# Performance work log

Hardware: AMD Instinct MI355X
Metric: run time of the kernel (lower is better)

The kernel has to match this reference:

```python
import jax, jax.numpy as jnp
import numpy as np

N_NODES = 100000
N_EDGES = 800000
F_IN = 300
F_PROJ = 256
HIDDEN = 256
F2 = 128
OUT = 4
NEG_SLOPE = 0.2
BN_EPS = 1e-5


def setup_inputs() -> dict:
    key = jax.random.key(0)
    ks = jax.random.split(key, 20)
    def g(k, shape, scale=0.05):
        return jax.random.normal(k, shape, dtype=jnp.float32) * scale
    return {
        "x": jax.random.normal(ks[0], (N_NODES, F_IN), dtype=jnp.float32),
        "edge_index": jax.random.randint(ks[1], (2, N_EDGES), 0, N_NODES),
        "lin_w": g(ks[2], (F_IN, F_PROJ)), "lin_b": jnp.zeros((F_PROJ,), jnp.float32),
        "w1_src": g(ks[3], (F_PROJ, HIDDEN)), "w1_dst": g(ks[4], (F_PROJ, HIDDEN)),
        "a1_src": g(ks[5], (HIDDEN,)), "a1_dst": g(ks[6], (HIDDEN,)),
        "b1": jnp.zeros((HIDDEN,), jnp.float32),
        "w2_src": g(ks[7], (HIDDEN, F2)), "w2_dst": g(ks[8], (HIDDEN, F2)),
        "a2_src": g(ks[9], (F2,)), "a2_dst": g(ks[10], (F2,)),
        "b2": jnp.zeros((F2,), jnp.float32),
        "fc1_w": g(ks[11], (F2, 64)), "fc1_b": jnp.zeros((64,), jnp.float32),
        "bn_g": jnp.ones((64,), jnp.float32), "bn_b": jnp.zeros((64,), jnp.float32),
        "fc2_w": g(ks[12], (64, OUT)), "fc2_b": jnp.zeros((OUT,), jnp.float32),
    }


def gat_conv(x, src, dst, w_src, w_dst, att_src, att_dst, bias, n):
    # PyG GATConv, heads=1: separate src/dst linear, additive attention, LeakyReLU,
    # per-destination segment softmax, weighted scatter-add aggregation.
    h_src = x @ w_src                      # [N, C]
    h_dst = x @ w_dst                      # [N, C]
    a_s = h_src @ att_src                  # [N]
    a_d = h_dst @ att_dst                  # [N]
    e = jax.nn.leaky_relu(a_s[src] + a_d[dst], NEG_SLOPE)  # [E]
    m = jax.ops.segment_max(e, dst, num_segments=n)
    w = jnp.exp(e - m[dst])
    denom = jax.ops.segment_sum(w, dst, num_segments=n)
    alpha = w / (denom[dst] + 1e-16)       # [E]
    out = jax.ops.segment_sum(h_src[src] * alpha[:, None], dst, num_segments=n)
    return out + bias


def reference(x, edge_index, lin_w, lin_b, w1_src, w1_dst, a1_src, a1_dst, b1,
              w2_src, w2_dst, a2_src, a2_dst, b2, fc1_w, fc1_b, bn_g, bn_b,
              fc2_w, fc2_b):
    n = x.shape[0]
    loops = jnp.arange(n)
    src = jnp.concatenate([edge_index[0], loops])  # add_self_loops=True (PyG default)
    dst = jnp.concatenate([edge_index[1], loops])
    h = jax.nn.relu(x @ lin_w + lin_b)             # node-type Linear(-1, 256) + relu
    h = jax.nn.relu(gat_conv(h, src, dst, w1_src, w1_dst, a1_src, a1_dst, b1, n))
    h = jax.nn.relu(gat_conv(h, src, dst, w2_src, w2_dst, a2_src, a2_dst, b2, n))
    h = h @ fc1_w + fc1_b
    mu = jnp.mean(h, axis=0)
    var = jnp.var(h, axis=0)
    h = (h - mu) * jax.lax.rsqrt(var + BN_EPS) * bn_g + bn_b
    h = jax.nn.relu(h)
    h = h @ fc2_w + fc2_b
    return jax.nn.log_softmax(h, axis=-1)
```

## Files before the change

### kernel.cpp

```cpp
#include <hip/hip_runtime.h>
#include <hip/hip_bf16.h>
#include <cmath>

#define NN 100000
#define NE 800000
#define ETOT (NE + NN)
#define MP 100096

#define SCHUNK 512
#define NBLK ((NN + SCHUNK - 1) / SCHUNK)

typedef __attribute__((ext_vector_type(8))) short bf16x8;
typedef __attribute__((ext_vector_type(4))) float f32x4;

__device__ inline void gl_lds16(const void* g, void* l) {
    __builtin_amdgcn_global_load_lds(
        (const __attribute__((address_space(1))) void*)g,
        (__attribute__((address_space(3))) void*)l, 16, 0, 0);
}

__device__ inline ushort f2bf(float f) {
    __hip_bfloat16 b = __float2bfloat16(f);
    return *(ushort*)&b;
}
__device__ inline uint pk2(float a, float b) {
    return (uint)f2bf(a) | ((uint)f2bf(b) << 16);
}

__global__ __launch_bounds__(256)
void mfma_gemm(const __hip_bfloat16* __restrict__ Abf,
               const __hip_bfloat16* __restrict__ Btbf,
               const float* __restrict__ bias, void* __restrict__ out,
               const float* __restrict__ dotv, float* __restrict__ dotout,
               float* __restrict__ stats,
               int Kp, int ldc, int Mstore, int Nstore, int flags)
{
    __shared__ __align__(16) short As[128 * 32];
    __shared__ __align__(16) short Bs[128 * 32];
    const short* A  = (const short*)Abf;
    const short* Bt = (const short*)Btbf;

    const int tid  = threadIdx.x;
    const int lane = tid & 63;
    const int wv   = tid >> 6;
    const int wr   = (wv >> 1) * 64;
    const int wc   = (wv & 1) * 64;
    const int quad = lane >> 4;
    const int l16  = lane & 15;
    const long bm = (long)blockIdx.x * 128;
    const long bn = (long)blockIdx.y * 128;

    const int r0 = tid >> 2;
    const int c0 = (tid & 3) ^ ((r0 >> 1) & 3);
    const int r1 = r0 + 64;
    const int c1 = (tid & 3) ^ ((r1 >> 1) & 3);
    const short* a_g0 = A + (bm + r0) * (long)Kp + c0 * 8;
    const short* a_g1 = A + (bm + r1) * (long)Kp + c1 * 8;
    const short* b_g0 = Bt + (bn + r0) * (long)Kp + c0 * 8;
    const short* b_g1 = Bt + (bn + r1) * (long)Kp + c1 * 8;
    short* a_l0 = &As[tid * 8];
    short* a_l1 = &As[(tid + 256) * 8];
    short* b_l0 = &Bs[tid * 8];
    short* b_l1 = &Bs[(tid + 256) * 8];

    f32x4 acc[4][4] = {};
    const int xr = (quad ^ ((l16 >> 1) & 3)) * 8;

    for (int k0 = 0; k0 < Kp; k0 += 32) {
        gl_lds16(a_g0 + k0, a_l0);
        gl_lds16(a_g1 + k0, a_l1);
        gl_lds16(b_g0 + k0, b_l0);
        gl_lds16(b_g1 + k0, b_l1);
        __syncthreads();

        bf16x8 af[4], bf[4];
#pragma unroll
        for (int i = 0; i < 4; i++)
            af[i] = *(const bf16x8*)&As[(wr + i * 16 + l16) * 32 + xr];
#pragma unroll
        for (int j = 0; j < 4; j++)
            bf[j] = *(const bf16x8*)&Bs[(wc + j * 16 + l16) * 32 + xr];
#pragma unroll
        for (int i = 0; i < 4; i++)
#pragma unroll
            for (int j = 0; j < 4; j++)
                acc[i][j] = __builtin_amdgcn_mfma_f32_16x16x32_bf16(
                    af[i], bf[j], acc[i][j], 0, 0, 0);
        __syncthreads();
    }

    __hip_bfloat16* outb = (__hip_bfloat16*)out;
    float* outf = (float*)out;
    float dp[16];
    float sv[4], sv2[4];
#pragma unroll
    for (int t = 0; t < 16; t++) dp[t] = 0.f;
#pragma unroll
    for (int j = 0; j < 4; j++) { sv[j] = 0.f; sv2[j] = 0.f; }

#pragma unroll
    for (int i = 0; i < 4; i++) {
        long row_base = bm + wr + i * 16 + quad * 4;
#pragma unroll
        for (int j = 0; j < 4; j++) {
            long col = bn + wc + j * 16 + l16;
            if (col >= Nstore) continue;
            float bv = bias ? bias[col] : 0.f;
            float dv = dotout ? dotv[col] : 0.f;
#pragma unroll
            for (int r = 0; r < 4; r++) {
                long row = row_base + r;
                float v = acc[i][j][r] + bv;
                if (flags & 1) v = fmaxf(v, 0.f);
                dp[i * 4 + r] = fmaf(v, dv, dp[i * 4 + r]);
                if (row >= Mstore) continue;
                if (flags & 4) { sv[j] += v; sv2[j] += v * v; }
                if (flags & 2) outb[row * ldc + col] = __float2bfloat16(v);
                else           outf[row * ldc + col] = v;
            }
        }
    }

    if (dotout) {
#pragma unroll
        for (int t = 0; t < 16; t++) {
            float s = dp[t];
            s += __shfl_xor(s, 1); s += __shfl_xor(s, 2);
            s += __shfl_xor(s, 4); s += __shfl_xor(s, 8);
            if (l16 == 0) {
                long row = bm + wr + (t >> 2) * 16 + quad * 4 + (t & 3);
                if (row < Mstore) atomicAdd(&dotout[row], s);
            }
        }
    }

    if (flags & 4) {
#pragma unroll
        for (int j = 0; j < 4; j++) {
            float s = sv[j], s2 = sv2[j];
            s  += __shfl_xor(s, 16);  s  += __shfl_xor(s, 32);
            s2 += __shfl_xor(s2, 16); s2 += __shfl_xor(s2, 32);
            if (quad == 0) {
                long col = bn + wc + j * 16 + l16;
                if (col < Nstore) {
                    atomicAdd(&stats[col], s);
                    atomicAdd(&stats[64 + col], s2);
                }
            }
        }
    }
}

__global__ __launch_bounds__(256)
void cast_x_vec(const float* __restrict__ x, __hip_bfloat16* __restrict__ xb)
{
    const int idx = blockIdx.x * 256 + threadIdx.x;
    if (idx >= MP * 40) return;
    const int row = idx / 40;
    const int c8  = (idx % 40) * 8;
    uint4 v;
    if (row < NN && c8 + 8 <= 300) {
        const float* xp = x + (size_t)row * 300 + c8;
        float4 f0 = *(const float4*)xp;
        float4 f1 = *(const float4*)(xp + 4);
        v.x = pk2(f0.x, f0.y); v.y = pk2(f0.z, f0.w);
        v.z = pk2(f1.x, f1.y); v.w = pk2(f1.z, f1.w);
    } else {
        float f[8];
#pragma unroll
        for (int k = 0; k < 8; k++)
            f[k] = (row < NN && c8 + k < 300) ? x[(size_t)row * 300 + c8 + k] : 0.f;
        v.x = pk2(f[0], f[1]); v.y = pk2(f[2], f[3]);
        v.z = pk2(f[4], f[5]); v.w = pk2(f[6], f[7]);
    }
    *(uint4*)((ushort*)xb + (size_t)row * 320 + c8) = v;
}

__device__ inline void castT_one(const float* __restrict__ w,
                                 __hip_bfloat16* __restrict__ wt,
                                 int K, int N, int Kp, int idx)
{
    int n = idx / Kp, k = idx % Kp;
    float v = (n < N && k < K) ? w[(size_t)k * N + n] : 0.f;
    wt[idx] = __float2bfloat16(v);
}

__global__ __launch_bounds__(256)
void prep_small(const float* __restrict__ lin_w, const float* __restrict__ w1_src,
                const float* __restrict__ w2_src, const float* __restrict__ fc1_w,
                const float* __restrict__ w1_dst, const float* __restrict__ a1_dst,
                const float* __restrict__ w2_dst, const float* __restrict__ a2_dst,
                __hip_bfloat16* __restrict__ wlinT, __hip_bfloat16* __restrict__ w1T,
                __hip_bfloat16* __restrict__ w2T, __hip_bfloat16* __restrict__ fc1T,
                float* __restrict__ vvec1, float* __restrict__ vvec2)
{
    const int b = blockIdx.x;
    const int tid = threadIdx.x;
    if (b < 320) {
        castT_one(lin_w, wlinT, 300, 256, 320, b * 256 + tid);
    } else if (b < 576) {
        castT_one(w1_src, w1T, 256, 256, 256, (b - 320) * 256 + tid);
    } else if (b < 704) {
        castT_one(w2_src, w2T, 256, 128, 256, (b - 576) * 256 + tid);
    } else if (b < 768) {
        castT_one(fc1_w, fc1T, 128, 64, 128, (b - 704) * 256 + tid);
    } else if (b == 768) {
        float s = 0.f;
        for (int j = 0; j < 256; j++) s = fmaf(w1_dst[(size_t)tid * 256 + j], a1_dst[j], s);
        vvec1[tid] = s;
    } else {
        float s = 0.f;
        for (int j = 0; j < 128; j++) s = fmaf(w2_dst[(size_t)tid * 128 + j], a2_dst[j], s);
        vvec2[tid] = s;
    }
}

__global__ void count_edges(const int* __restrict__ ei, int* __restrict__ counts)
{
    int e = blockIdx.x * blockDim.x + threadIdx.x;
    if (e >= ETOT) return;
    int d = (e < NE) ? ei[NE + e] : (e - NE);
    atomicAdd(&counts[d], 1);
}

__global__ __launch_bounds__(256)
void scan_partial(const int* __restrict__ counts, int* __restrict__ blk)
{
    __shared__ int sh[256];
    const int tid = threadIdx.x;
    const int base = blockIdx.x * SCHUNK + tid * 2;
    int c0 = (base < NN)     ? counts[base]     : 0;
    int c1 = (base + 1 < NN) ? counts[base + 1] : 0;
    sh[tid] = c0 + c1;
    __syncthreads();
    for (int off = 128; off; off >>= 1) {
        if (tid < off) sh[tid] += sh[tid + off];
        __syncthreads();
    }
    if (tid == 0) blk[blockIdx.x] = sh[0];
}

__global__ __launch_bounds__(256)
void scan_blocks(int* __restrict__ blk)
{
    __shared__ int sh[256];
    const int tid = threadIdx.x;
    int v = (tid < NBLK) ? blk[tid] : 0;
    sh[tid] = v;
    __syncthreads();
    for (int off = 1; off < 256; off <<= 1) {
        int u = (tid >= off) ? sh[tid - off] : 0;
        __syncthreads();
        sh[tid] += u;
        __syncthreads();
    }
    if (tid < NBLK) blk[tid] = sh[tid] - v;
}

__global__ __launch_bounds__(256)
void scan_fill(const int* __restrict__ counts, const int* __restrict__ blk,
               int* __restrict__ row_ptr, int* __restrict__ cursor)
{
    __shared__ int sh[256];
    const int tid = threadIdx.x;
    const int i0 = blockIdx.x * SCHUNK + tid * 2;
    int c0 = (i0 < NN)     ? counts[i0]     : 0;
    int c1 = (i0 + 1 < NN) ? counts[i0 + 1] : 0;
    int s = c0 + c1;
    sh[tid] = s;
    __syncthreads();
    for (int off = 1; off < 256; off <<= 1) {
        int u = (tid >= off) ? sh[tid - off] : 0;
        __syncthreads();
        sh[tid] += u;
        __syncthreads();
    }
    int pre = sh[tid] - s + blk[blockIdx.x];
    if (i0 < NN)     { row_ptr[i0] = pre;          cursor[i0] = pre; }
    if (i0 + 1 < NN) { row_ptr[i0 + 1] = pre + c0; cursor[i0 + 1] = pre + c0; }
    if (blockIdx.x == 0 && tid == 0) row_ptr[NN] = ETOT;
}

__global__ void fill_edges(const int* __restrict__ ei, int* __restrict__ cursor,
                           int* __restrict__ csr_src)
{
    int e = blockIdx.x * blockDim.x + threadIdx.x;
    if (e >= ETOT) return;
    int s, d;
    if (e < NE) { s = ei[e]; d = ei[NE + e]; }
    else        { s = e - NE; d = s; }
    int pos = atomicAdd(&cursor[d], 1);
    csr_src[pos] = s;
}

template<int LPN>
__global__ __launch_bounds__(256)
void gat_agg_wave(const __hip_bfloat16* __restrict__ hsrc,
                  const float* __restrict__ a_s,
                  const float* __restrict__ a_d,
                  const int* __restrict__ row_ptr,
                  const int* __restrict__ csr_src,
                  const float* __restrict__ bias,
                  __hip_bfloat16* __restrict__ outh,
                  const float* __restrict__ dotv,
                  float* __restrict__ dotout)
{
    const int C = LPN * 4;
    const int NPB = 256 / LPN;
    __shared__ __align__(16) float2 ws_sh[NPB][LPN];

    const int tid  = threadIdx.x;
    const int slot = tid / LPN;
    const int sub  = tid % LPN;
    const int n = blockIdx.x * NPB + slot;
    if (n >= NN) return;

    const int start = row_ptr[n];
    const int deg = row_ptr[n + 1] - start;
    const float a_dn = a_d[n];
    const ushort* hp = (const ushort*)hsrc;

    float S = 0.f;
    float acc0 = 0.f, acc1 = 0.f, acc2 = 0.f, acc3 = 0.f;

    for (int c0 = 0; c0 < deg; c0 += LPN) {
        const int cnt = min(LPN, deg - c0);
        int sj = 0; float w = 0.f;
        if (sub < cnt) {
            sj = csr_src[start + c0 + sub];
            float t = a_s[sj] + a_dn;
            t = (t >= 0.f) ? t : 0.2f * t;
            w = __expf(t);
        }
        S += w;
        ws_sh[slot][sub] = make_float2(w, __int_as_float(sj));

        const int cnt8 = (cnt + 7) & ~7;
        const ushort* hpl = hp + sub * 4;
        for (int j = 0; j < cnt8; j += 8) {
            float4 p0 = *(const float4*)&ws_sh[slot][j];
            float4 p1 = *(const float4*)&ws_sh[slot][j + 2];
            float4 p2 = *(const float4*)&ws_sh[slot][j + 4];
            float4 p3 = *(const float4*)&ws_sh[slot][j + 6];
            uint2 u0 = *(const uint2*)(hpl + (size_t)__float_as_int(p0.y) * C);
            uint2 u1 = *(const uint2*)(hpl + (size_t)__float_as_int(p0.w) * C);
            uint2 u2 = *(const uint2*)(hpl + (size_t)__float_as_int(p1.y) * C);
            uint2 u3 = *(const uint2*)(hpl + (size_t)__float_as_int(p1.w) * C);
            uint2 u4 = *(const uint2*)(hpl + (size_t)__float_as_int(p2.y) * C);
            uint2 u5 = *(const uint2*)(hpl + (size_t)__float_as_int(p2.w) * C);
            uint2 u6 = *(const uint2*)(hpl + (size_t)__float_as_int(p3.y) * C);
            uint2 u7 = *(const uint2*)(hpl + (size_t)__float_as_int(p3.w) * C);
#define ACC4(W, U) \
            acc0 = fmaf(W, __uint_as_float(U.x << 16), acc0); \
            acc1 = fmaf(W, __uint_as_float(U.x & 0xffff0000u), acc1); \
            acc2 = fmaf(W, __uint_as_float(U.y << 16), acc2); \
            acc3 = fmaf(W, __uint_as_float(U.y & 0xffff0000u), acc3);
            ACC4(p0.x, u0) ACC4(p0.z, u1) ACC4(p1.x, u2) ACC4(p1.z, u3)
            ACC4(p2.x, u4) ACC4(p2.z, u5) ACC4(p3.x, u6) ACC4(p3.z, u7)
#undef ACC4
        }
    }

#pragma unroll
    for (int off = LPN / 2; off; off >>= 1) S += __shfl_xor(S, off);

    float inv = 1.f / (S + 1e-16f);
    const float4 b4 = *(const float4*)&bias[sub * 4];
    float o0 = fmaxf(acc0 * inv + b4.x, 0.f);
    float o1 = fmaxf(acc1 * inv + b4.y, 0.f);
    float o2 = fmaxf(acc2 * inv + b4.z, 0.f);
    float o3 = fmaxf(acc3 * inv + b4.w, 0.f);

    ushort4 v;
    v.x = f2bf(o0); v.y = f2bf(o1); v.z = f2bf(o2); v.w = f2bf(o3);
    *(ushort4*)((ushort*)outh + (size_t)n * C + sub * 4) = v;

    if (dotout) {
        const float4 d4 = *(const float4*)&dotv[sub * 4];
        float dp = o0 * d4.x + o1 * d4.y + o2 * d4.z + o3 * d4.w;
#pragma unroll
        for (int off = LPN / 2; off; off >>= 1) dp += __shfl_xor(dp, off);
        if (sub == 0) dotout[n] = dp;
    }
}

__global__ void bn_finalize(const float* __restrict__ stats,
                            const float* __restrict__ g, const float* __restrict__ b,
                            float* __restrict__ ss)
{
    int c = threadIdx.x;
    float mu = stats[c] / (float)NN;
    float var = stats[64 + c] / (float)NN - mu * mu;
    float rs = rsqrtf(var + 1e-5f);
    float sc = rs * g[c];
    ss[c] = sc;
    ss[64 + c] = b[c] - mu * sc;
}

__global__ __launch_bounds__(256)
void final_head(const float* __restrict__ h3, const float* __restrict__ ss,
                const float* __restrict__ fc2_w, const float* __restrict__ fc2_b,
                float* __restrict__ out)
{
    int lane = threadIdx.x & 63;
    int n = blockIdx.x * 4 + (threadIdx.x >> 6);
    if (n >= NN) return;
    float y = h3[(size_t)n * 64 + lane];
    y = fmaxf(y * ss[lane] + ss[64 + lane], 0.f);
    float z[4];
#pragma unroll
    for (int o = 0; o < 4; o++) {
        float p = y * fc2_w[lane * 4 + o];
#pragma unroll
        for (int off = 32; off; off >>= 1) p += __shfl_xor(p, off);
        z[o] = p + fc2_b[o];
    }
    float mx = fmaxf(fmaxf(z[0], z[1]), fmaxf(z[2], z[3]));
    float lse = mx + logf(expf(z[0] - mx) + expf(z[1] - mx) +
                          expf(z[2] - mx) + expf(z[3] - mx));
    if (lane < 4) out[(size_t)n * 4 + lane] = z[lane] - lse;
}

extern "C" void kernel_launch(void* const* d_in, const int* in_sizes, int n_in,
                              void* d_out, int out_size, void* d_ws, size_t ws_size,
                              hipStream_t stream)
{
    const float* x      = (const float*)d_in[0];
    const int*   ei     = (const int*)d_in[1];
    const float* lin_w  = (const float*)d_in[2];
    const float* lin_b  = (const float*)d_in[3];
    const float* w1_src = (const float*)d_in[4];
    const float* w1_dst = (const float*)d_in[5];
    const float* a1_src = (const float*)d_in[6];
    const float* a1_dst = (const float*)d_in[7];
    const float* b1     = (const float*)d_in[8];
    const float* w2_src = (const float*)d_in[9];
    const float* w2_dst = (const float*)d_in[10];
    const float* a2_src = (const float*)d_in[11];
    const float* a2_dst = (const float*)d_in[12];
    const float* b2     = (const float*)d_in[13];
    const float* fc1_w  = (const float*)d_in[14];
    const float* fc1_b  = (const float*)d_in[15];
    const float* bn_g   = (const float*)d_in[16];
    const float* bn_b   = (const float*)d_in[17];
    const float* fc2_w  = (const float*)d_in[18];
    const float* fc2_b  = (const float*)d_in[19];
    float* out = (float*)d_out;

    char* p = (char*)d_ws;
    auto alloc = [&](size_t bytes) { char* r = p; p += (bytes + 255) & ~(size_t)255; return r; };
    char* R1 = alloc((size_t)MP * 320 * 2);
    char* R2 = alloc((size_t)MP * 256 * 2);
    char* R3 = alloc((size_t)MP * 256 * 2);
    __hip_bfloat16* wlinT = (__hip_bfloat16*)alloc(256 * 320 * 2);
    __hip_bfloat16* w1T   = (__hip_bfloat16*)alloc(256 * 256 * 2);
    __hip_bfloat16* w2T   = (__hip_bfloat16*)alloc(128 * 256 * 2);
    __hip_bfloat16* fc1T  = (__hip_bfloat16*)alloc(128 * 128 * 2);
    float* avec  = (float*)alloc((size_t)NN * 4 * 4 + 512);
    float* aS1 = avec;
    float* aD1 = avec + NN;
    float* aS2 = avec + 2 * (size_t)NN;
    float* aD2 = avec + 3 * (size_t)NN;
    float* stats = avec + 4 * (size_t)NN;
    float* vvec1 = (float*)alloc(256 * 4);
    float* vvec2 = (float*)alloc(256 * 4);
    float* ss    = (float*)alloc(128 * 4);
    int* row_ptr = (int*)alloc((size_t)(NN + 1) * 4);
    int* cursor  = (int*)alloc((size_t)(NN + 1) * 4);
    int* counts  = (int*)alloc((size_t)NN * 4);
    int* blk     = (int*)alloc(256 * 4);
    int* csr_src = (int*)alloc((size_t)ETOT * 4);

    __hip_bfloat16* x_bf  = (__hip_bfloat16*)R1;
    __hip_bfloat16* hsrc1 = (__hip_bfloat16*)R1;
    __hip_bfloat16* h0    = (__hip_bfloat16*)R2;
    __hip_bfloat16* hsrc2 = (__hip_bfloat16*)R2;
    __hip_bfloat16* h2    = (__hip_bfloat16*)(R2 + (size_t)MP * 128 * 2);
    __hip_bfloat16* h1    = (__hip_bfloat16*)R3;
    float*          h3    = (float*)R3;

    const int eb = (ETOT + 255) / 256;
    const int MB = MP / 128;

    hipMemsetAsync(avec, 0, sizeof(float) * NN * 4 + 512, stream);

    hipMemsetAsync(counts, 0, sizeof(int) * NN, stream);
    count_edges<<<eb, 256, 0, stream>>>(ei, counts);
    scan_partial<<<NBLK, 256, 0, stream>>>(counts, blk);
    scan_blocks<<<1, 256, 0, stream>>>(blk);
    scan_fill<<<NBLK, 256, 0, stream>>>(counts, blk, row_ptr, cursor);
    fill_edges<<<eb, 256, 0, stream>>>(ei, cursor, csr_src);

    cast_x_vec<<<(MP * 40 + 255) / 256, 256, 0, stream>>>(x, x_bf);
    prep_small<<<770, 256, 0, stream>>>(lin_w, w1_src, w2_src, fc1_w,
                                        w1_dst, a1_dst, w2_dst, a2_dst,
                                        wlinT, w1T, w2T, fc1T, vvec1, vvec2);

    mfma_gemm<<<dim3(MB, 2), 256, 0, stream>>>(x_bf, wlinT, lin_b, h0,
                                               vvec1, aD1, nullptr, 320, 256, NN, 256, 3);

    mfma_gemm<<<dim3(MB, 2), 256, 0, stream>>>(h0, w1T, nullptr, hsrc1,
                                               a1_src, aS1, nullptr, 256, 256, NN, 256, 2);
    gat_agg_wave<64><<<(NN + 3) / 4, 256, 0, stream>>>(hsrc1, aS1, aD1, row_ptr,
                                                       csr_src, b1, h1, vvec2, aD2);

    mfma_gemm<<<dim3(MB, 1), 256, 0, stream>>>(h1, w2T, nullptr, hsrc2,
                                               a2_src, aS2, nullptr, 256, 128, NN, 128, 2);
    gat_agg_wave<32><<<(NN + 7) / 8, 256, 0, stream>>>(hsrc2, aS2, aD2, row_ptr,
                                                       csr_src, b2, h2, nullptr, nullptr);

    mfma_gemm<<<dim3(MB, 1), 256, 0, stream>>>(h2, fc1T, fc1_b, h3,
                                               nullptr, nullptr, stats, 128, 64, NN, 64, 4);
    bn_finalize<<<1, 64, 0, stream>>>(stats, bn_g, bn_b, ss);
    final_head<<<(NN + 3) / 4, 256, 0, stream>>>(h3, ss, fc2_w, fc2_b, out);
}
```

Measured before the change: 699.4 us.

## Restructure GEMM to stage only B panels in LDS and read A directly

Replaces the 128x128x32 LDS-tiled GEMM with a panel kernel. It loads a 128-row by 128-K slice of the weight matrix into LDS with an XOR swizzle, and each wave reads its 32 rows of A straight from global memory into registers. The goal is fewer barriers per K step and no LDS staging of the large activation matrix. In exchange, A reads become uncoalesced per-lane 16-byte global loads, and LDS use grows to 32KB, which may reduce occupancy.

```diff
diff --git a/kernel.cpp b/kernel.cpp
--- a/kernel.cpp
+++ b/kernel.cpp
@@ -28,91 +28,84 @@
 }
 
 __global__ __launch_bounds__(256)
-void mfma_gemm(const __hip_bfloat16* __restrict__ Abf,
-               const __hip_bfloat16* __restrict__ Btbf,
-               const float* __restrict__ bias, void* __restrict__ out,
-               const float* __restrict__ dotv, float* __restrict__ dotout,
-               float* __restrict__ stats,
-               int Kp, int ldc, int Mstore, int Nstore, int flags)
-{
-    __shared__ __align__(16) short As[128 * 32];
-    __shared__ __align__(16) short Bs[128 * 32];
+void gemm_panel(const __hip_bfloat16* __restrict__ Abf,
+                const __hip_bfloat16* __restrict__ Btbf,
+                const float* __restrict__ bias, void* __restrict__ out,
+                const float* __restrict__ dotv, float* __restrict__ dotout,
+                float* __restrict__ stats,
+                int Kp, int ldc, int Mstore, int Nstore, int flags)
+{
+    __shared__ __align__(16) short Bs[128 * 128];
     const short* A  = (const short*)Abf;
     const short* Bt = (const short*)Btbf;
 
     const int tid  = threadIdx.x;
     const int lane = tid & 63;
     const int wv   = tid >> 6;
-    const int wr   = (wv >> 1) * 64;
-    const int wc   = (wv & 1) * 64;
     const int quad = lane >> 4;
     const int l16  = lane & 15;
     const long bm = (long)blockIdx.x * 128;
     const long bn = (long)blockIdx.y * 128;
 
-    const int r0 = tid >> 2;
-    const int c0 = (tid & 3) ^ ((r0 >> 1) & 3);
-    const int r1 = r0 + 64;
-    const int c1 = (tid & 3) ^ ((r1 >> 1) & 3);
-    const short* a_g0 = A + (bm + r0) * (long)Kp + c0 * 8;
-    const short* a_g1 = A + (bm + r1) * (long)Kp + c1 * 8;
-    const short* b_g0 = Bt + (bn + r0) * (long)Kp + c0 * 8;
-    const short* b_g1 = Bt + (bn + r1) * (long)Kp + c1 * 8;
-    short* a_l0 = &As[tid * 8];
-    short* a_l1 = &As[(tid + 256) * 8];
-    short* b_l0 = &Bs[tid * 8];
-    short* b_l1 = &Bs[(tid + 256) * 8];
-
-    f32x4 acc[4][4] = {};
-    const int xr = (quad ^ ((l16 >> 1) & 3)) * 8;
-
-    for (int k0 = 0; k0 < Kp; k0 += 32) {
-        gl_lds16(a_g0 + k0, a_l0);
-        gl_lds16(a_g1 + k0, a_l1);
-        gl_lds16(b_g0 + k0, b_l0);
-        gl_lds16(b_g1 + k0, b_l1);
+    f32x4 acc[2][8] = {};
+
+    const short* a_row0 = A + (bm + wv * 32 + l16) * (long)Kp;
+    const short* a_row1 = a_row0 + 16 * (long)Kp;
+
+    for (int k0 = 0; k0 < Kp; k0 += 128) {
+        const int nc   = min(16, (Kp - k0) >> 3);
+        const int mask = nc - 1;
+        const int sh   = (nc == 16) ? 4 : 3;
+
+        if (k0 > 0) __syncthreads();
+        const int slots = 128 * nc;
+        for (int i = 0; i < slots; i += 256) {
+            int s = i + tid;
+            int row = s >> sh;
+            int cslot = s & mask;
+            int gc = cslot ^ (row & mask);
+            gl_lds16(Bt + (bn + row) * (long)Kp + k0 + gc * 8, &Bs[s * 8]);
+        }
         __syncthreads();
 
-        bf16x8 af[4], bf[4];
-#pragma unroll
-        for (int i = 0; i < 4; i++)
-            af[i] = *(const bf16x8*)&As[(wr + i * 16 + l16) * 32 + xr];
-#pragma unroll
-        for (int j = 0; j < 4; j++)
-            bf[j] = *(const bf16x8*)&Bs[(wc + j * 16 + l16) * 32 + xr];
-#pragma unroll
-        for (int i = 0; i < 4; i++)
-#pragma unroll
-            for (int j = 0; j < 4; j++)
-                acc[i][j] = __builtin_amdgcn_mfma_f32_16x16x32_bf16(
-                    af[i], bf[j], acc[i][j], 0, 0, 0);
-        __syncthreads();
+        const int nkk = nc >> 2;
+        const int cxor = l16 & mask;
+#pragma unroll 4
+        for (int kk = 0; kk < nkk; kk++) {
+            bf16x8 a0 = *(const bf16x8*)(a_row0 + k0 + kk * 32 + quad * 8);
+            bf16x8 a1 = *(const bf16x8*)(a_row1 + k0 + kk * 32 + quad * 8);
+            const int cs = (kk * 4 + quad) ^ cxor;
+#pragma unroll
+            for (int j = 0; j < 8; j++) {
+                bf16x8 bfj = *(const bf16x8*)&Bs[(j * 16 + l16) * (nc * 8) + cs * 8];
+                acc[0][j] = __builtin_amdgcn_mfma_f32_16x16x32_bf16(a0, bfj, acc[0][j], 0, 0, 0);
+                acc[1][j] = __builtin_amdgcn_mfma_f32_16x16x32_bf16(a1, bfj, acc[1][j], 0, 0, 0);
+            }
+        }
     }
 
     __hip_bfloat16* outb = (__hip_bfloat16*)out;
     float* outf = (float*)out;
-    float dp[16];
-    float sv[4], sv2[4];
-#pragma unroll
-    for (int t = 0; t < 16; t++) dp[t] = 0.f;
-#pragma unroll
-    for (int j = 0; j < 4; j++) { sv[j] = 0.f; sv2[j] = 0.f; }
-
-#pragma unroll
-    for (int i = 0; i < 4; i++) {
-        long row_base = bm + wr + i * 16 + quad * 4;
-#pragma unroll
-        for (int j = 0; j < 4; j++) {
-            long col = bn + wc + j * 16 + l16;
+    float dp[8];
+    float sv[8], sv2[8];
+#pragma unroll
+    for (int t = 0; t < 8; t++) { dp[t] = 0.f; sv[t] = 0.f; sv2[t] = 0.f; }
+
+#pragma unroll
+    for (int rt = 0; rt < 2; rt++) {
+        long row_base = bm + wv * 32 + rt * 16 + quad * 4;
+#pragma unroll
+        for (int j = 0; j < 8; j++) {
+            long col = bn + j * 16 + l16;
             if (col >= Nstore) continue;
             float bv = bias ? bias[col] : 0.f;
             float dv = dotout ? dotv[col] : 0.f;
 #pragma unroll
             for (int r = 0; r < 4; r++) {
                 long row = row_base + r;
-                float v = acc[i][j][r] + bv;
+                float v = acc[rt][j][r] + bv;
                 if (flags & 1) v = fmaxf(v, 0.f);
-                dp[i * 4 + r] = fmaf(v, dv, dp[i * 4 + r]);
+                dp[rt * 4 + r] = fmaf(v, dv, dp[rt * 4 + r]);
                 if (row >= Mstore) continue;
                 if (flags & 4) { sv[j] += v; sv2[j] += v * v; }
                 if (flags & 2) outb[row * ldc + col] = __float2bfloat16(v);
@@ -123,12 +116,12 @@
 
     if (dotout) {
 #pragma unroll
-        for (int t = 0; t < 16; t++) {
+        for (int t = 0; t < 8; t++) {
             float s = dp[t];
             s += __shfl_xor(s, 1); s += __shfl_xor(s, 2);
             s += __shfl_xor(s, 4); s += __shfl_xor(s, 8);
             if (l16 == 0) {
-                long row = bm + wr + (t >> 2) * 16 + quad * 4 + (t & 3);
+                long row = bm + wv * 32 + (t >> 2) * 16 + quad * 4 + (t & 3);
                 if (row < Mstore) atomicAdd(&dotout[row], s);
             }
         }
@@ -136,16 +129,15 @@
 
     if (flags & 4) {
 #pragma unroll
-        for (int j = 0; j < 4; j++) {
+        for (int j = 0; j < 8; j++) {
+            long col = bn + j * 16 + l16;
+            if (col >= Nstore) continue;
             float s = sv[j], s2 = sv2[j];
             s  += __shfl_xor(s, 16);  s  += __shfl_xor(s, 32);
             s2 += __shfl_xor(s2, 16); s2 += __shfl_xor(s2, 32);
             if (quad == 0) {
-                long col = bn + wc + j * 16 + l16;
-                if (col < Nstore) {
-                    atomicAdd(&stats[col], s);
-                    atomicAdd(&stats[64 + col], s2);
-                }
+                atomicAdd(&stats[col], s);
+                atomicAdd(&stats[64 + col], s2);
             }
         }
     }
@@ -496,21 +488,21 @@
                                         w1_dst, a1_dst, w2_dst, a2_dst,
                                         wlinT, w1T, w2T, fc1T, vvec1, vvec2);
 
-    mfma_gemm<<<dim3(MB, 2), 256, 0, stream>>>(x_bf, wlinT, lin_b, h0,
-                                               vvec1, aD1, nullptr, 320, 256, NN, 256, 3);
-
-    mfma_gemm<<<dim3(MB, 2), 256, 0, stream>>>(h0, w1T, nullptr, hsrc1,
-                                               a1_src, aS1, nullptr, 256, 256, NN, 256, 2);
+    gemm_panel<<<dim3(MB, 2), 256, 0, stream>>>(x_bf, wlinT, lin_b, h0,
+                                                vvec1, aD1, nullptr, 320, 256, NN, 256, 3);
+
+    gemm_panel<<<dim3(MB, 2), 256, 0, stream>>>(h0, w1T, nullptr, hsrc1,
+                                                a1_src, aS1, nullptr, 256, 256, NN, 256, 2);
     gat_agg_wave<64><<<(NN + 3) / 4, 256, 0, stream>>>(hsrc1, aS1, aD1, row_ptr,
                                                        csr_src, b1, h1, vvec2, aD2);
 
-    mfma_gemm<<<dim3(MB, 1), 256, 0, stream>>>(h1, w2T, nullptr, hsrc2,
-                                               a2_src, aS2, nullptr, 256, 128, NN, 128, 2);
+    gemm_panel<<<dim3(MB, 1), 256, 0, stream>>>(h1, w2T, nullptr, hsrc2,
+                                                a2_src, aS2, nullptr, 256, 128, NN, 128, 2);
     gat_agg_wave<32><<<(NN + 7) / 8, 256, 0, stream>>>(hsrc2, aS2, aD2, row_ptr,
                                                        csr_src, b2, h2, nullptr, nullptr);
 
-    mfma_gemm<<<dim3(MB, 1), 256, 0, stream>>>(h2, fc1T, fc1_b, h3,
-                                               nullptr, nullptr, stats, 128, 64, NN, 64, 4);
+    gemm_panel<<<dim3(MB, 1), 256, 0, stream>>>(h2, fc1T, fc1_b, h3,
+                                                nullptr, nullptr, stats, 128, 64, NN, 64, 4);
     bn_finalize<<<1, 64, 0, stream>>>(stats, bn_g, bn_b, ss);
     final_head<<<(NN + 3) / 4, 256, 0, stream>>>(h3, ss, fc2_w, fc2_b, out);
 }
```

After: 736.5 us. 1.05x slower.

## Double-buffer LDS tiles in MFMA GEMM to overlap loads with compute

Applied to the files above, without the earlier changes.

The GEMM kernel now keeps two LDS buffers for the A and B tiles. While the current K-slice runs through the MFMA instructions, the async global-to-LDS loads for the next slice are already in flight. This removes one barrier per iteration and is meant to hide global load latency behind compute. In exchange it doubles the shared memory per block, which may lower occupancy.

```diff
diff --git a/kernel.cpp b/kernel.cpp
--- a/kernel.cpp
+++ b/kernel.cpp
@@ -35,8 +35,8 @@
                float* __restrict__ stats,
                int Kp, int ldc, int Mstore, int Nstore, int flags)
 {
-    __shared__ __align__(16) short As[128 * 32];
-    __shared__ __align__(16) short Bs[128 * 32];
+    __shared__ __align__(16) short As[2][128 * 32];
+    __shared__ __align__(16) short Bs[2][128 * 32];
     const short* A  = (const short*)Abf;
     const short* Bt = (const short*)Btbf;
 
@@ -58,35 +58,42 @@
     const short* a_g1 = A + (bm + r1) * (long)Kp + c1 * 8;
     const short* b_g0 = Bt + (bn + r0) * (long)Kp + c0 * 8;
     const short* b_g1 = Bt + (bn + r1) * (long)Kp + c1 * 8;
-    short* a_l0 = &As[tid * 8];
-    short* a_l1 = &As[(tid + 256) * 8];
-    short* b_l0 = &Bs[tid * 8];
-    short* b_l1 = &Bs[(tid + 256) * 8];
 
     f32x4 acc[4][4] = {};
     const int xr = (quad ^ ((l16 >> 1) & 3)) * 8;
-
-    for (int k0 = 0; k0 < Kp; k0 += 32) {
-        gl_lds16(a_g0 + k0, a_l0);
-        gl_lds16(a_g1 + k0, a_l1);
-        gl_lds16(b_g0 + k0, b_l0);
-        gl_lds16(b_g1 + k0, b_l1);
+    const int nIter = Kp >> 5;
+
+    {
+        gl_lds16(a_g0, &As[0][tid * 8]);
+        gl_lds16(a_g1, &As[0][(tid + 256) * 8]);
+        gl_lds16(b_g0, &Bs[0][tid * 8]);
+        gl_lds16(b_g1, &Bs[0][(tid + 256) * 8]);
+    }
+
+    for (int it = 0; it < nIter; it++) {
         __syncthreads();
-
+        const int nb = (it + 1) & 1;
+        if (it + 1 < nIter) {
+            const int k = (it + 1) * 32;
+            gl_lds16(a_g0 + k, &As[nb][tid * 8]);
+            gl_lds16(a_g1 + k, &As[nb][(tid + 256) * 8]);
+            gl_lds16(b_g0 + k, &Bs[nb][tid * 8]);
+            gl_lds16(b_g1 + k, &Bs[nb][(tid + 256) * 8]);
+        }
+        const int cb = it & 1;
         bf16x8 af[4], bf[4];
 #pragma unroll
         for (int i = 0; i < 4; i++)
-            af[i] = *(const bf16x8*)&As[(wr + i * 16 + l16) * 32 + xr];
+            af[i] = *(const bf16x8*)&As[cb][(wr + i * 16 + l16) * 32 + xr];
 #pragma unroll
         for (int j = 0; j < 4; j++)
-            bf[j] = *(const bf16x8*)&Bs[(wc + j * 16 + l16) * 32 + xr];
+            bf[j] = *(const bf16x8*)&Bs[cb][(wc + j * 16 + l16) * 32 + xr];
 #pragma unroll
         for (int i = 0; i < 4; i++)
 #pragma unroll
             for (int j = 0; j < 4; j++)
                 acc[i][j] = __builtin_amdgcn_mfma_f32_16x16x32_bf16(
                     af[i], bf[j], acc[i][j], 0, 0, 0);
-        __syncthreads();
     }
 
     __hip_bfloat16* outb = (__hip_bfloat16*)out;
```

New measurement: 698.8 us. No clear change (-0.1%).
